# Optimization experiments

Hardware: AMD Instinct MI355X
Metric: run time of the kernel (lower is better)

Reference implementation:

```python
import jax, jax.numpy as jnp
import numpy as np
import math

EPS_NORM = 1e-6
EPS_COS = 1e-6


def _rms_norm(x, scale, eps):
    ms = jnp.mean(jnp.square(x), axis=-1, keepdims=True)
    return x * (scale * jax.lax.rsqrt(ms + eps))


def _apply_rope(x, theta):
    # x: [n, nh, s, e], theta: [n, nh, s, d] with 2*d <= e
    d = theta.shape[-1]
    x1, x2, rest = x[..., :d], x[..., d:2 * d], x[..., 2 * d:]
    cos, sin = jnp.cos(theta), jnp.sin(theta)
    y1 = x1 * cos - x2 * sin
    y2 = x2 * cos + x1 * sin
    return jnp.concatenate([y1, y2, rest], axis=-1)


def _make_freqs(d_head, n_heads):
    dim = d_head // 2
    log_min, log_max = math.log(math.pi), math.log(10.0 * math.pi)
    f = np.exp(np.linspace(log_min, log_max, n_heads * dim // 4 + 1, dtype=np.float64)[:-1])
    return jnp.asarray(f.reshape(dim // 4, n_heads).T, dtype=jnp.float32)  # [n_heads, dim//4]


def setup_inputs() -> dict:
    key = jax.random.key(0)
    ks = jax.random.split(key, 8)
    n, H, W, d_model = 4, 32, 32, 1024
    d_head, n_heads, cond_f = 64, 16, 1024
    x = jax.random.normal(ks[0], (n, H, W, d_model), dtype=jnp.float32)
    pos = jax.random.uniform(ks[1], (n, H, W, 2), dtype=jnp.float32) * 2.0 - 1.0
    cond = jax.random.normal(ks[2], (n, cond_f), dtype=jnp.float32)
    norm_scale = jnp.ones((d_model,), dtype=jnp.float32)
    ada_w = jax.random.normal(ks[3], (3 * d_model, cond_f), dtype=jnp.float32) * 0.02
    ada_b = jnp.zeros((3 * d_model,), dtype=jnp.float32)
    qkv_w = jax.random.normal(ks[4], (3 * d_model, d_model), dtype=jnp.float32) * 0.02
    attn_scale = jnp.full((n_heads,), 10.0, dtype=jnp.float32)
    out_w = jax.random.normal(ks[5], (d_model, d_model), dtype=jnp.float32) * 0.02
    freqs = _make_freqs(d_head, n_heads)
    return {"x": x, "pos": pos, "cond": cond, "norm_scale": norm_scale,
            "ada_w": ada_w, "ada_b": ada_b, "qkv_w": qkv_w,
            "attn_scale": attn_scale, "out_w": out_w, "freqs": freqs}


def reference(x, pos, cond, norm_scale, ada_w, ada_b, qkv_w, attn_scale, out_w, freqs):
    n, H, W, d_model = x.shape
    n_heads, nf = freqs.shape          # nf = d_head//4... actually (d_head//2)//4
    d_head = d_model // n_heads
    s = H * W
    skip = x
    # adaLN modulation
    mod = jax.nn.silu(cond) @ ada_w.T + ada_b              # [n, 3*d_model]
    shift, scale, gate = jnp.split(mod, 3, axis=-1)        # each [n, d_model]
    xn = _rms_norm(x, norm_scale, EPS_NORM)
    xm = xn * (1.0 + scale[:, None, None, :]) + shift[:, None, None, :]
    # qkv projection: layout (t nh e) on last dim
    qkv = (xm @ qkv_w.T).reshape(n, s, 3, n_heads, d_head)
    q, k, v = qkv[:, :, 0], qkv[:, :, 1], qkv[:, :, 2]     # [n, s, nh, e]
    q = jnp.transpose(q, (0, 2, 1, 3))                     # [n, nh, s, e]
    k = jnp.transpose(k, (0, 2, 1, 3))
    v = jnp.transpose(v, (0, 2, 1, 3))
    # cosine-sim scaling per head
    sqrt_scale = jnp.sqrt(attn_scale)[None, :, None, None]
    q = q * (sqrt_scale * jax.lax.rsqrt(jnp.sum(jnp.square(q), axis=-1, keepdims=True) + EPS_COS))
    k = k * (sqrt_scale * jax.lax.rsqrt(jnp.sum(jnp.square(k), axis=-1, keepdims=True) + EPS_COS))
    # axial RoPE angles
    posf = pos.reshape(n, s, 2)
    theta_h = posf[:, :, None, 0:1] * freqs                # [n, s, nh, nf]
    theta_w = posf[:, :, None, 1:2] * freqs
    theta = jnp.concatenate([theta_h, theta_w], axis=-1)   # [n, s, nh, 2*nf]
    theta = jnp.transpose(theta, (0, 2, 1, 3))             # [n, nh, s, 2*nf]
    q = _apply_rope(q, theta)
    k = _apply_rope(k, theta)
    # attention with softmax scale 1.0 (cosine-sim already scaled)
    scores = jnp.einsum('bnse,bnte->bnst', q, k)
    attn = jax.nn.softmax(scores, axis=-1)
    o = jnp.einsum('bnst,bnte->bnse', attn, v)             # [n, nh, s, e]
    o = jnp.transpose(o, (0, 2, 1, 3)).reshape(n, H, W, d_model)
    o = o @ out_w.T
    return skip + gate[:, None, None, :] * o
```

## Files before the change

kernel.cpp:

```cpp
#include <hip/hip_runtime.h>
#include <stdint.h>

typedef __bf16 bf16x8 __attribute__((ext_vector_type(8)));
typedef uint16_t u16x8 __attribute__((ext_vector_type(8)));
typedef float f32x4 __attribute__((ext_vector_type(4)));

#define DEV static __device__ __forceinline__

DEV uint16_t f2bf(float f) {
  union { float f; uint32_t u; } v; v.f = f;
  return (uint16_t)((v.u + 0x8000u) >> 16);
}
DEV float bf2f(uint16_t h) {
  union { uint32_t u; float f; } v; v.u = ((uint32_t)h) << 16;
  return v.f;
}

#define GLOAD_LDS16(g, l)                                                     \
  __builtin_amdgcn_global_load_lds(                                           \
      (__attribute__((address_space(1))) void*)(g),                           \
      (__attribute__((address_space(3))) void*)(l), 16, 0, 0)

__global__ void k_conv(const float* __restrict__ src, uint16_t* __restrict__ dst, int n) {
  int i = blockIdx.x * blockDim.x + threadIdx.x;
  int stride = gridDim.x * blockDim.x;
  for (; i < n; i += stride) dst[i] = f2bf(src[i]);
}

__global__ void k_mod(const float* __restrict__ cond, const float* __restrict__ ada_w,
                      const float* __restrict__ ada_b, float* __restrict__ mod) {
  int w = threadIdx.x >> 6, lane = threadIdx.x & 63;
  int gid = blockIdx.x * 4 + w;
  int b = gid / 3072, j = gid - b * 3072;
  const float* cw = cond + b * 1024;
  const float* aw = ada_w + (size_t)j * 1024;
  float sum = 0.f;
  for (int i = 0; i < 16; ++i) {
    int f = lane + (i << 6);
    float c = cw[f];
    float sc = c / (1.f + __expf(-c));
    sum += sc * aw[f];
  }
  for (int m = 32; m; m >>= 1) sum += __shfl_xor(sum, m, 64);
  if (lane == 0) mod[b * 3072 + j] = sum + ada_b[j];
}

__global__ void k_norm_mod(const float* __restrict__ x, const float* __restrict__ norm_scale,
                           const float* __restrict__ mod, uint16_t* __restrict__ xm) {
  int row = blockIdx.x;
  int b = row >> 10;
  const float* xr = x + (size_t)row * 1024;
  const float* shiftp = mod + b * 3072;
  const float* scalep = shiftp + 1024;
  int t = threadIdx.x;
  float v[4];
  float s = 0.f;
  for (int i = 0; i < 4; ++i) { v[i] = xr[t + (i << 8)]; s += v[i] * v[i]; }
  for (int m = 32; m; m >>= 1) s += __shfl_xor(s, m, 64);
  __shared__ float red[4];
  if ((t & 63) == 0) red[t >> 6] = s;
  __syncthreads();
  s = red[0] + red[1] + red[2] + red[3];
  float inv = rsqrtf(s * (1.f / 1024.f) + 1e-6f);
  uint16_t* xo = xm + (size_t)row * 1024;
  for (int i = 0; i < 4; ++i) {
    int c = t + (i << 8);
    float val = v[i] * inv * norm_scale[c];
    val = val * (1.f + scalep[c]) + shiftp[c];
    xo[c] = f2bf(val);
  }
}

template <int N, int EPI>
__global__ __launch_bounds__(256) void k_gemm(const uint16_t* __restrict__ A,
                                              const uint16_t* __restrict__ B,
                                              uint16_t* __restrict__ Cbf,
                                              const float* __restrict__ skip,
                                              const float* __restrict__ modp,
                                              float* __restrict__ Cout) {
  constexpr int K = 1024;
  __shared__ uint16_t As[128 * 32];
  __shared__ uint16_t Bs[128 * 32];
  int t = threadIdx.x;
  int lane = t & 63;
  int w = t >> 6, wr = w >> 1, wc = w & 1;
  int bm = blockIdx.y, bn = blockIdx.x;
  f32x4 acc[4][4] = {};
  const size_t a_base = (size_t)(bm * 128) * K;
  const size_t b_base = (size_t)(bn * 128) * K;
  int r = t >> 2, cch = t & 3;
  for (int kt = 0; kt < K / 32; ++kt) {
    __syncthreads();
#pragma unroll
    for (int i = 0; i < 2; ++i) {
      int rr = r + (i << 6);
      int cs = (cch ^ ((rr >> 1) & 3)) << 3;
      GLOAD_LDS16(A + a_base + (size_t)rr * K + kt * 32 + cs, As + rr * 32 + (cch << 3));
      GLOAD_LDS16(B + b_base + (size_t)rr * K + kt * 32 + cs, Bs + rr * 32 + (cch << 3));
    }
    __syncthreads();
    bf16x8 af[4], bfr[4];
    int lq = lane >> 4;
#pragma unroll
    for (int m = 0; m < 4; ++m) {
      int R = wr * 64 + m * 16 + (lane & 15);
      af[m] = *reinterpret_cast<const bf16x8*>(&As[R * 32 + ((lq ^ ((R >> 1) & 3)) << 3)]);
    }
#pragma unroll
    for (int n = 0; n < 4; ++n) {
      int R = wc * 64 + n * 16 + (lane & 15);
      bfr[n] = *reinterpret_cast<const bf16x8*>(&Bs[R * 32 + ((lq ^ ((R >> 1) & 3)) << 3)]);
    }
#pragma unroll
    for (int m = 0; m < 4; ++m)
#pragma unroll
      for (int n = 0; n < 4; ++n)
        acc[m][n] = __builtin_amdgcn_mfma_f32_16x16x32_bf16(af[m], bfr[n], acc[m][n], 0, 0, 0);
  }
  int row0 = bm * 128 + wr * 64;
  int col0 = bn * 128 + wc * 64;
#pragma unroll
  for (int m = 0; m < 4; ++m)
#pragma unroll
    for (int n = 0; n < 4; ++n)
#pragma unroll
      for (int rr = 0; rr < 4; ++rr) {
        int R = row0 + m * 16 + ((lane >> 4) << 2) + rr;
        int C = col0 + n * 16 + (lane & 15);
        float v = acc[m][n][rr];
        if (EPI == 0) {
          Cbf[(size_t)R * N + C] = f2bf(v);
        } else {
          float g = modp[(R >> 10) * 3072 + 2048 + C];
          Cout[(size_t)R * N + C] = skip[(size_t)R * N + C] + g * v;
        }
      }
}

__global__ __launch_bounds__(256) void k_qkvpost(
    const uint16_t* __restrict__ qkv, const float* __restrict__ pos,
    const float* __restrict__ freqs, const float* __restrict__ attn_scale,
    uint16_t* __restrict__ Qb, uint16_t* __restrict__ Kb, uint16_t* __restrict__ Vt) {
  __shared__ uint16_t vtile[64 * 66];
  int t = threadIdx.x;
  int st = blockIdx.x, bh = blockIdx.y;
  int b = bh >> 4, h = bh & 15;
  int r = t >> 2;
  int s = t & 3;
  int sp = st * 64 + r;
  size_t m = (size_t)b * 1024 + sp;
  const uint16_t* basep = qkv + m * 3072 + h * 64 + s * 16;
  bf16x8 q0 = *reinterpret_cast<const bf16x8*>(basep);
  bf16x8 q1 = *reinterpret_cast<const bf16x8*>(basep + 8);
  bf16x8 k0 = *reinterpret_cast<const bf16x8*>(basep + 1024);
  bf16x8 k1 = *reinterpret_cast<const bf16x8*>(basep + 1032);
  u16x8 v0 = *reinterpret_cast<const u16x8*>(basep + 2048);
  u16x8 v1 = *reinterpret_cast<const u16x8*>(basep + 2056);
  float qv[16], kv[16];
#pragma unroll
  for (int i = 0; i < 8; ++i) {
    qv[i] = (float)q0[i]; qv[8 + i] = (float)q1[i];
    kv[i] = (float)k0[i]; kv[8 + i] = (float)k1[i];
  }
  float sq = 0.f, sk = 0.f;
#pragma unroll
  for (int i = 0; i < 16; ++i) { sq += qv[i] * qv[i]; sk += kv[i] * kv[i]; }
  sq += __shfl_xor(sq, 1, 64); sq += __shfl_xor(sq, 2, 64);
  sk += __shfl_xor(sk, 1, 64); sk += __shfl_xor(sk, 2, 64);
  float ss = sqrtf(attn_scale[h]);
  float qs = ss * rsqrtf(sq + 1e-6f);
  float ks = ss * rsqrtf(sk + 1e-6f);
#pragma unroll
  for (int i = 0; i < 16; ++i) { qv[i] *= qs; kv[i] *= ks; }
  float p0 = pos[m * 2], p1 = pos[m * 2 + 1];
  float sgn = (s == 0) ? -1.f : 1.f;
#pragma unroll
  for (int i = 0; i < 16; ++i) {
    float pq = __shfl_xor(qv[i], 1, 64);
    float pk = __shfl_xor(kv[i], 1, 64);
    if (s < 2) {
      float th = ((i < 8) ? p0 : p1) * freqs[h * 8 + (i & 7)];
      float sn, cs;
      __sincosf(th, &sn, &cs);
      qv[i] = qv[i] * cs + sgn * pq * sn;
      kv[i] = kv[i] * cs + sgn * pk * sn;
    }
  }
  bf16x8 qo0, qo1, ko0, ko1;
#pragma unroll
  for (int i = 0; i < 8; ++i) {
    qo0[i] = (__bf16)qv[i]; qo1[i] = (__bf16)qv[8 + i];
    ko0[i] = (__bf16)kv[i]; ko1[i] = (__bf16)kv[8 + i];
  }
  size_t qkb = ((size_t)bh * 1024 + sp) * 64 + s * 16;
  *reinterpret_cast<bf16x8*>(Qb + qkb) = qo0;
  *reinterpret_cast<bf16x8*>(Qb + qkb + 8) = qo1;
  *reinterpret_cast<bf16x8*>(Kb + qkb) = ko0;
  *reinterpret_cast<bf16x8*>(Kb + qkb + 8) = ko1;
#pragma unroll
  for (int i = 0; i < 8; ++i) {
    vtile[(s * 16 + i) * 66 + r] = v0[i];
    vtile[(s * 16 + 8 + i) * 66 + r] = v1[i];
  }
  __syncthreads();
  int d = t >> 2, c = t & 3;
  u16x8 w0, w1;
#pragma unroll
  for (int i = 0; i < 8; ++i) {
    w0[i] = vtile[d * 66 + c * 16 + i];
    w1[i] = vtile[d * 66 + c * 16 + 8 + i];
  }
  size_t vb = ((size_t)bh * 64 + d) * 1024 + st * 64 + c * 16;
  *reinterpret_cast<u16x8*>(Vt + vb) = w0;
  *reinterpret_cast<u16x8*>(Vt + vb + 8) = w1;
}

__global__ __launch_bounds__(512) void k_attn(const uint16_t* __restrict__ Qb,
                                              const uint16_t* __restrict__ Kb,
                                              const uint16_t* __restrict__ Vt,
                                              uint16_t* __restrict__ obuf) {
  __shared__ uint16_t Ks[64 * 64];
  __shared__ uint16_t Vs[64 * 64];
  __shared__ uint16_t Ps[8][16 * 88];
  int t = threadIdx.x, lane = t & 63, w = t >> 6;
  int qt = blockIdx.y, bh = blockIdx.x;
  int b = bh >> 4, h = bh & 15;
  int qrow = qt * 128 + w * 16 + (lane & 15);
  int klo = (lane >> 4) << 3;
  const uint16_t* qptr = Qb + ((size_t)bh * 1024 + qrow) * 64 + klo;
  bf16x8 qf0 = *reinterpret_cast<const bf16x8*>(qptr);
  bf16x8 qf1 = *reinterpret_cast<const bf16x8*>(qptr + 32);
  f32x4 oacc[4] = {};
  float denom[4] = {0.f, 0.f, 0.f, 0.f};
  const size_t kbase = (size_t)bh * 1024 * 64;
  const size_t vbase = (size_t)bh * 64 * 1024;
  for (int kt = 0; kt < 16; ++kt) {
    __syncthreads();
    {
      int row = t >> 3;
      int ce = ((t & 7) ^ (row & 7)) << 3;
      GLOAD_LDS16(Kb + kbase + (size_t)(kt * 64 + row) * 64 + ce, Ks + t * 8);
      GLOAD_LDS16(Vt + vbase + (size_t)row * 1024 + kt * 64 + ce, Vs + t * 8);
    }
    __syncthreads();
    bf16x8 pa0, pa1;
    {
      f32x4 s[4];
      for (int n = 0; n < 4; ++n) {
        int row = n * 16 + (lane & 15);
        int sw = (row & 7) << 3;
        bf16x8 kf0 = *reinterpret_cast<const bf16x8*>(&Ks[row * 64 + (klo ^ sw)]);
        bf16x8 kf1 = *reinterpret_cast<const bf16x8*>(&Ks[row * 64 + ((32 + klo) ^ sw)]);
        f32x4 z = {};
        z = __builtin_amdgcn_mfma_f32_16x16x32_bf16(qf0, kf0, z, 0, 0, 0);
        z = __builtin_amdgcn_mfma_f32_16x16x32_bf16(qf1, kf1, z, 0, 0, 0);
        s[n] = z;
      }
      for (int n = 0; n < 4; ++n)
        for (int rr = 0; rr < 4; ++rr) {
          float p = __expf(s[n][rr]);
          denom[rr] += p;
          Ps[w][(((lane >> 4) << 2) + rr) * 88 + n * 16 + (lane & 15)] = f2bf(p);
        }
      pa0 = *reinterpret_cast<const bf16x8*>(&Ps[w][(lane & 15) * 88 + klo]);
      pa1 = *reinterpret_cast<const bf16x8*>(&Ps[w][(lane & 15) * 88 + 32 + klo]);
    }
    for (int dt = 0; dt < 4; ++dt) {
      int row = dt * 16 + (lane & 15);
      int sw = (row & 7) << 3;
      bf16x8 vf0 = *reinterpret_cast<const bf16x8*>(&Vs[row * 64 + (klo ^ sw)]);
      bf16x8 vf1 = *reinterpret_cast<const bf16x8*>(&Vs[row * 64 + ((32 + klo) ^ sw)]);
      oacc[dt] = __builtin_amdgcn_mfma_f32_16x16x32_bf16(pa0, vf0, oacc[dt], 0, 0, 0);
      oacc[dt] = __builtin_amdgcn_mfma_f32_16x16x32_bf16(pa1, vf1, oacc[dt], 0, 0, 0);
    }
  }
  for (int rr = 0; rr < 4; ++rr)
    for (int msk = 8; msk; msk >>= 1) denom[rr] += __shfl_xor(denom[rr], msk, 64);
  for (int rr = 0; rr < 4; ++rr) {
    float rinv = 1.f / denom[rr];
    int sp = qt * 128 + w * 16 + ((lane >> 4) << 2) + rr;
    size_t orow = ((size_t)b * 1024 + sp) * 1024 + h * 64;
    for (int dt = 0; dt < 4; ++dt)
      obuf[orow + dt * 16 + (lane & 15)] = f2bf(oacc[dt][rr] * rinv);
  }
}

extern "C" void kernel_launch(void* const* d_in, const int* in_sizes, int n_in,
                              void* d_out, int out_size, void* d_ws, size_t ws_size,
                              hipStream_t stream) {
  const float* x = (const float*)d_in[0];
  const float* pos = (const float*)d_in[1];
  const float* cond = (const float*)d_in[2];
  const float* norm_scale = (const float*)d_in[3];
  const float* ada_w = (const float*)d_in[4];
  const float* ada_b = (const float*)d_in[5];
  const float* qkv_w = (const float*)d_in[6];
  const float* attn_scale = (const float*)d_in[7];
  const float* out_w = (const float*)d_in[8];
  const float* freqs = (const float*)d_in[9];
  float* out = (float*)d_out;
  char* ws = (char*)d_ws;
  float* mod = (float*)(ws + 0);
  uint16_t* xm = (uint16_t*)(ws + 65536);
  uint16_t* qkvw_bf = (uint16_t*)(ws + 8454144);
  uint16_t* outw_bf = (uint16_t*)(ws + 14745600);
  uint16_t* qkv = (uint16_t*)(ws + 16842752);
  uint16_t* Qb = (uint16_t*)(ws + 42008576);
  uint16_t* Kb = (uint16_t*)(ws + 50397184);
  uint16_t* Vt = (uint16_t*)(ws + 58785792);
  uint16_t* obuf = (uint16_t*)(ws + 67174400);

  k_conv<<<dim3(1024), dim3(256), 0, stream>>>(qkv_w, qkvw_bf, 3 * 1024 * 1024);
  k_conv<<<dim3(512), dim3(256), 0, stream>>>(out_w, outw_bf, 1024 * 1024);
  k_mod<<<dim3(3072), dim3(256), 0, stream>>>(cond, ada_w, ada_b, mod);
  k_norm_mod<<<dim3(4096), dim3(256), 0, stream>>>(x, norm_scale, mod, xm);
  k_gemm<3072, 0><<<dim3(24, 32), dim3(256), 0, stream>>>(xm, qkvw_bf, qkv, nullptr, nullptr, nullptr);
  k_qkvpost<<<dim3(16, 64), dim3(256), 0, stream>>>(qkv, pos, freqs, attn_scale, Qb, Kb, Vt);
  k_attn<<<dim3(64, 8), dim3(512), 0, stream>>>(Qb, Kb, Vt, obuf);
  k_gemm<1024, 1><<<dim3(8, 32), dim3(256), 0, stream>>>(obuf, outw_bf, nullptr, x, mod, out);
}
```

Before: 124.4 us.

## Replace QKV GEMM with 256x256-tile double-buffered pipelined MFMA kernel

Adds a dedicated QKV projection GEMM that uses 256x256 output tiles, 512 threads and BK=64. Operand tiles are double-buffered in LDS with an XOR swizzle and loaded through direct global-to-LDS loads. The loads are spread across four compute phases with explicit waitcnt, barriers and setprio, so memory traffic overlaps MFMA work and each loaded tile is reused more. The cost is only 192 workgroups, fewer than the CU count, a large LDS footprint and hand-tuned synchronization.

```diff
diff --git a/kernel.cpp b/kernel.cpp
--- a/kernel.cpp
+++ b/kernel.cpp
@@ -69,6 +69,114 @@
     val = val * (1.f + scalep[c]) + shiftp[c];
     xo[c] = f2bf(val);
   }
+}
+
+__global__ __launch_bounds__(512) void k_gemm256(const uint16_t* __restrict__ A,
+                                                 const uint16_t* __restrict__ B,
+                                                 uint16_t* __restrict__ Cbf) {
+  constexpr int K = 1024;
+  constexpr int NT = 16;
+  constexpr int NCOL = 3072;
+  __shared__ uint16_t As[2][256 * 64];
+  __shared__ uint16_t Bs[2][256 * 64];
+  const int t = threadIdx.x;
+  const int lane = t & 63;
+  const int w = t >> 6;
+  const int wr = w >> 2;
+  const int wc = w & 3;
+  const int bm = blockIdx.y, bn = blockIdx.x;
+  const size_t a_base = (size_t)(bm * 256) * K;
+  const size_t b_base = (size_t)(bn * 256) * K;
+  const int sr = t >> 3;
+  const int sc = t & 7;
+
+  f32x4 acc[8][4] = {};
+
+  auto stage = [&](const uint16_t* __restrict__ G, size_t gbase, uint16_t* lds,
+                   int kt, int half) {
+#pragma unroll
+    for (int j = 0; j < 2; ++j) {
+      int row = (half << 7) + (j << 6) + sr;
+      int scs = sc ^ (row & 7);
+      GLOAD_LDS16(G + gbase + (size_t)row * K + kt * 64 + (scs << 3),
+                  lds + (row << 6) + (sc << 3));
+    }
+  };
+
+#define PHASE(MB, STAGE_STMT, GATE_STMT)                                       \
+  {                                                                            \
+    STAGE_STMT;                                                                \
+    bf16x8 af[2][2];                                                           \
+    _Pragma("unroll") for (int mi = 0; mi < 2; ++mi) {                         \
+      int R = wr * 128 + (MB + mi) * 16 + (lane & 15);                         \
+      _Pragma("unroll") for (int kk = 0; kk < 2; ++kk)                         \
+          af[mi][kk] = *reinterpret_cast<const bf16x8*>(                       \
+              &Ac[(R << 6) + ((((kk << 2) + (lane >> 4)) ^ (R & 7)) << 3)]);   \
+    }                                                                          \
+    __builtin_amdgcn_s_barrier();                                              \
+    __builtin_amdgcn_sched_barrier(0);                                         \
+    __builtin_amdgcn_s_setprio(1);                                             \
+    _Pragma("unroll") for (int mi = 0; mi < 2; ++mi)                           \
+        _Pragma("unroll") for (int n = 0; n < 4; ++n) {                        \
+      acc[MB + mi][n] = __builtin_amdgcn_mfma_f32_16x16x32_bf16(               \
+          af[mi][0], bfr[n][0], acc[MB + mi][n], 0, 0, 0);                     \
+      acc[MB + mi][n] = __builtin_amdgcn_mfma_f32_16x16x32_bf16(               \
+          af[mi][1], bfr[n][1], acc[MB + mi][n], 0, 0, 0);                     \
+    }                                                                          \
+    __builtin_amdgcn_s_setprio(0);                                             \
+    GATE_STMT;                                                                 \
+    __builtin_amdgcn_s_barrier();                                              \
+    __builtin_amdgcn_sched_barrier(0);                                         \
+  }
+
+  stage(B, b_base, Bs[0], 0, 0);
+  stage(B, b_base, Bs[0], 0, 1);
+  stage(A, a_base, As[0], 0, 0);
+  stage(A, a_base, As[0], 0, 1);
+  stage(B, b_base, Bs[1], 1, 0);
+  stage(B, b_base, Bs[1], 1, 1);
+  asm volatile("s_waitcnt vmcnt(4)" ::: "memory");
+  __builtin_amdgcn_s_barrier();
+  __builtin_amdgcn_sched_barrier(0);
+
+  for (int kt = 0; kt < NT; ++kt) {
+    const int cur = kt & 1;
+    const uint16_t* __restrict__ Ac = As[cur];
+    const uint16_t* __restrict__ Bc = Bs[cur];
+    uint16_t* An = As[cur ^ 1];
+    uint16_t* Bn = Bs[cur];
+
+    if (kt + 1 < NT) stage(A, a_base, An, kt + 1, 0);
+    bf16x8 bfr[4][2];
+#pragma unroll
+    for (int n = 0; n < 4; ++n) {
+      int R = wc * 64 + n * 16 + (lane & 15);
+#pragma unroll
+      for (int kk = 0; kk < 2; ++kk)
+        bfr[n][kk] = *reinterpret_cast<const bf16x8*>(
+            &Bc[(R << 6) + ((((kk << 2) + (lane >> 4)) ^ (R & 7)) << 3)]);
+    }
+    PHASE(0, , )
+    PHASE(2, if (kt + 1 < NT) stage(A, a_base, An, kt + 1, 1), )
+    PHASE(4, if (kt + 2 < NT) stage(B, b_base, Bn, kt + 2, 0), )
+    PHASE(6, if (kt + 2 < NT) stage(B, b_base, Bn, kt + 2, 1),
+          if (kt < NT - 2) asm volatile("s_waitcnt vmcnt(4)" ::: "memory");
+          else asm volatile("s_waitcnt vmcnt(0)" ::: "memory"))
+  }
+#undef PHASE
+
+  const int row0 = bm * 256 + wr * 128;
+  const int col0 = bn * 256 + wc * 64;
+#pragma unroll
+  for (int m = 0; m < 8; ++m)
+#pragma unroll
+    for (int n = 0; n < 4; ++n)
+#pragma unroll
+      for (int rr = 0; rr < 4; ++rr) {
+        int R = row0 + m * 16 + ((lane >> 4) << 2) + rr;
+        int C = col0 + n * 16 + (lane & 15);
+        Cbf[(size_t)R * NCOL + C] = f2bf(acc[m][n][rr]);
+      }
 }
 
 template <int N, int EPI>
@@ -314,7 +422,7 @@
   k_conv<<<dim3(512), dim3(256), 0, stream>>>(out_w, outw_bf, 1024 * 1024);
   k_mod<<<dim3(3072), dim3(256), 0, stream>>>(cond, ada_w, ada_b, mod);
   k_norm_mod<<<dim3(4096), dim3(256), 0, stream>>>(x, norm_scale, mod, xm);
-  k_gemm<3072, 0><<<dim3(24, 32), dim3(256), 0, stream>>>(xm, qkvw_bf, qkv, nullptr, nullptr, nullptr);
+  k_gemm256<<<dim3(12, 16), dim3(512), 0, stream>>>(xm, qkvw_bf, qkv);
   k_qkvpost<<<dim3(16, 64), dim3(256), 0, stream>>>(qkv, pos, freqs, attn_scale, Qb, Kb, Vt);
   k_attn<<<dim3(64, 8), dim3(512), 0, stream>>>(Qb, Kb, Vt, obuf);
   k_gemm<1024, 1><<<dim3(8, 32), dim3(256), 0, stream>>>(obuf, outw_bf, nullptr, x, mod, out);
```

Measured after the change: 141.1 us. 1.13x slower.

## Process two query sub-tiles per wave in attention to reuse K/V fragments

Applied to the files above, without the earlier changes.

The attention kernel moves from 8 waves of 16 query rows to 4 waves of 32 query rows per block, so each wave computes two 16-row query sub-tiles. Each K and V fragment read from LDS is reused for two MFMA groups, halving LDS reads per MFMA, and the K/V tile loads are split across the smaller thread count. In exchange, register pressure per thread rises from the doubled accumulators and scores, there are fewer waves per block to hide latency, and the loops are now explicitly unrolled.

```diff
diff --git a/kernel.cpp b/kernel.cpp
--- a/kernel.cpp
+++ b/kernel.cpp
@@ -215,74 +215,100 @@
   *reinterpret_cast<u16x8*>(Vt + vb + 8) = w1;
 }
 
-__global__ __launch_bounds__(512) void k_attn(const uint16_t* __restrict__ Qb,
+__global__ __launch_bounds__(256) void k_attn(const uint16_t* __restrict__ Qb,
                                               const uint16_t* __restrict__ Kb,
                                               const uint16_t* __restrict__ Vt,
                                               uint16_t* __restrict__ obuf) {
   __shared__ uint16_t Ks[64 * 64];
   __shared__ uint16_t Vs[64 * 64];
-  __shared__ uint16_t Ps[8][16 * 88];
+  __shared__ uint16_t Ps[4][32 * 88];
   int t = threadIdx.x, lane = t & 63, w = t >> 6;
   int qt = blockIdx.y, bh = blockIdx.x;
   int b = bh >> 4, h = bh & 15;
-  int qrow = qt * 128 + w * 16 + (lane & 15);
   int klo = (lane >> 4) << 3;
-  const uint16_t* qptr = Qb + ((size_t)bh * 1024 + qrow) * 64 + klo;
-  bf16x8 qf0 = *reinterpret_cast<const bf16x8*>(qptr);
-  bf16x8 qf1 = *reinterpret_cast<const bf16x8*>(qptr + 32);
-  f32x4 oacc[4] = {};
-  float denom[4] = {0.f, 0.f, 0.f, 0.f};
+  bf16x8 qf[2][2];
+#pragma unroll
+  for (int qs = 0; qs < 2; ++qs) {
+    int qrow = qt * 128 + w * 32 + qs * 16 + (lane & 15);
+    const uint16_t* qptr = Qb + ((size_t)bh * 1024 + qrow) * 64 + klo;
+    qf[qs][0] = *reinterpret_cast<const bf16x8*>(qptr);
+    qf[qs][1] = *reinterpret_cast<const bf16x8*>(qptr + 32);
+  }
+  f32x4 oacc[2][4] = {};
+  float denom[2][4] = {};
   const size_t kbase = (size_t)bh * 1024 * 64;
   const size_t vbase = (size_t)bh * 64 * 1024;
   for (int kt = 0; kt < 16; ++kt) {
     __syncthreads();
-    {
-      int row = t >> 3;
-      int ce = ((t & 7) ^ (row & 7)) << 3;
-      GLOAD_LDS16(Kb + kbase + (size_t)(kt * 64 + row) * 64 + ce, Ks + t * 8);
-      GLOAD_LDS16(Vt + vbase + (size_t)row * 1024 + kt * 64 + ce, Vs + t * 8);
+#pragma unroll
+    for (int i = 0; i < 2; ++i) {
+      int slot = t + (i << 8);
+      int row = slot >> 3;
+      int ce = ((slot & 7) ^ (row & 7)) << 3;
+      GLOAD_LDS16(Kb + kbase + (size_t)(kt * 64 + row) * 64 + ce, Ks + slot * 8);
+      GLOAD_LDS16(Vt + vbase + (size_t)row * 1024 + kt * 64 + ce, Vs + slot * 8);
     }
     __syncthreads();
-    bf16x8 pa0, pa1;
-    {
-      f32x4 s[4];
-      for (int n = 0; n < 4; ++n) {
-        int row = n * 16 + (lane & 15);
-        int sw = (row & 7) << 3;
-        bf16x8 kf0 = *reinterpret_cast<const bf16x8*>(&Ks[row * 64 + (klo ^ sw)]);
-        bf16x8 kf1 = *reinterpret_cast<const bf16x8*>(&Ks[row * 64 + ((32 + klo) ^ sw)]);
+    f32x4 s[2][4];
+#pragma unroll
+    for (int n = 0; n < 4; ++n) {
+      int row = n * 16 + (lane & 15);
+      int sw = (row & 7) << 3;
+      bf16x8 kf0 = *reinterpret_cast<const bf16x8*>(&Ks[row * 64 + (klo ^ sw)]);
+      bf16x8 kf1 = *reinterpret_cast<const bf16x8*>(&Ks[row * 64 + ((32 + klo) ^ sw)]);
+#pragma unroll
+      for (int qs = 0; qs < 2; ++qs) {
         f32x4 z = {};
-        z = __builtin_amdgcn_mfma_f32_16x16x32_bf16(qf0, kf0, z, 0, 0, 0);
-        z = __builtin_amdgcn_mfma_f32_16x16x32_bf16(qf1, kf1, z, 0, 0, 0);
-        s[n] = z;
+        z = __builtin_amdgcn_mfma_f32_16x16x32_bf16(qf[qs][0], kf0, z, 0, 0, 0);
+        z = __builtin_amdgcn_mfma_f32_16x16x32_bf16(qf[qs][1], kf1, z, 0, 0, 0);
+        s[qs][n] = z;
       }
+    }
+#pragma unroll
+    for (int qs = 0; qs < 2; ++qs)
+#pragma unroll
       for (int n = 0; n < 4; ++n)
+#pragma unroll
         for (int rr = 0; rr < 4; ++rr) {
-          float p = __expf(s[n][rr]);
-          denom[rr] += p;
-          Ps[w][(((lane >> 4) << 2) + rr) * 88 + n * 16 + (lane & 15)] = f2bf(p);
+          float p = __expf(s[qs][n][rr]);
+          denom[qs][rr] += p;
+          Ps[w][(qs * 16 + ((lane >> 4) << 2) + rr) * 88 + n * 16 + (lane & 15)] = f2bf(p);
         }
-      pa0 = *reinterpret_cast<const bf16x8*>(&Ps[w][(lane & 15) * 88 + klo]);
-      pa1 = *reinterpret_cast<const bf16x8*>(&Ps[w][(lane & 15) * 88 + 32 + klo]);
-    }
+    bf16x8 pa[2][2];
+#pragma unroll
+    for (int qs = 0; qs < 2; ++qs) {
+      pa[qs][0] = *reinterpret_cast<const bf16x8*>(&Ps[w][(qs * 16 + (lane & 15)) * 88 + klo]);
+      pa[qs][1] = *reinterpret_cast<const bf16x8*>(&Ps[w][(qs * 16 + (lane & 15)) * 88 + 32 + klo]);
+    }
+#pragma unroll
     for (int dt = 0; dt < 4; ++dt) {
       int row = dt * 16 + (lane & 15);
       int sw = (row & 7) << 3;
       bf16x8 vf0 = *reinterpret_cast<const bf16x8*>(&Vs[row * 64 + (klo ^ sw)]);
       bf16x8 vf1 = *reinterpret_cast<const bf16x8*>(&Vs[row * 64 + ((32 + klo) ^ sw)]);
-      oacc[dt] = __builtin_amdgcn_mfma_f32_16x16x32_bf16(pa0, vf0, oacc[dt], 0, 0, 0);
-      oacc[dt] = __builtin_amdgcn_mfma_f32_16x16x32_bf16(pa1, vf1, oacc[dt], 0, 0, 0);
-    }
-  }
-  for (int rr = 0; rr < 4; ++rr)
-    for (int msk = 8; msk; msk >>= 1) denom[rr] += __shfl_xor(denom[rr], msk, 64);
-  for (int rr = 0; rr < 4; ++rr) {
-    float rinv = 1.f / denom[rr];
-    int sp = qt * 128 + w * 16 + ((lane >> 4) << 2) + rr;
-    size_t orow = ((size_t)b * 1024 + sp) * 1024 + h * 64;
-    for (int dt = 0; dt < 4; ++dt)
-      obuf[orow + dt * 16 + (lane & 15)] = f2bf(oacc[dt][rr] * rinv);
-  }
+#pragma unroll
+      for (int qs = 0; qs < 2; ++qs) {
+        oacc[qs][dt] = __builtin_amdgcn_mfma_f32_16x16x32_bf16(pa[qs][0], vf0, oacc[qs][dt], 0, 0, 0);
+        oacc[qs][dt] = __builtin_amdgcn_mfma_f32_16x16x32_bf16(pa[qs][1], vf1, oacc[qs][dt], 0, 0, 0);
+      }
+    }
+  }
+#pragma unroll
+  for (int qs = 0; qs < 2; ++qs)
+#pragma unroll
+    for (int rr = 0; rr < 4; ++rr)
+      for (int msk = 8; msk; msk >>= 1) denom[qs][rr] += __shfl_xor(denom[qs][rr], msk, 64);
+#pragma unroll
+  for (int qs = 0; qs < 2; ++qs)
+#pragma unroll
+    for (int rr = 0; rr < 4; ++rr) {
+      float rinv = 1.f / denom[qs][rr];
+      int sp = qt * 128 + w * 32 + qs * 16 + ((lane >> 4) << 2) + rr;
+      size_t orow = ((size_t)b * 1024 + sp) * 1024 + h * 64;
+#pragma unroll
+      for (int dt = 0; dt < 4; ++dt)
+        obuf[orow + dt * 16 + (lane & 15)] = f2bf(oacc[qs][dt][rr] * rinv);
+    }
 }
 
 extern "C" void kernel_launch(void* const* d_in, const int* in_sizes, int n_in,
@@ -316,6 +342,6 @@
   k_norm_mod<<<dim3(4096), dim3(256), 0, stream>>>(x, norm_scale, mod, xm);
   k_gemm<3072, 0><<<dim3(24, 32), dim3(256), 0, stream>>>(xm, qkvw_bf, qkv, nullptr, nullptr, nullptr);
   k_qkvpost<<<dim3(16, 64), dim3(256), 0, stream>>>(qkv, pos, freqs, attn_scale, Qb, Kb, Vt);
-  k_attn<<<dim3(64, 8), dim3(512), 0, stream>>>(Qb, Kb, Vt, obuf);
+  k_attn<<<dim3(64, 8), dim3(256), 0, stream>>>(Qb, Kb, Vt, obuf);
   k_gemm<1024, 1><<<dim3(8, 32), dim3(256), 0, stream>>>(obuf, outw_bf, nullptr, x, mod, out);
 }
```

Result: no change. 124.8 us (+0.3%).
